# Kernel optimization log

Hardware: AMD Instinct MI355X
Metric: run time of the kernel (lower is better)

## Reference

```python
import jax, jax.numpy as jnp
import numpy as np

B, S, D, H = 8, 1024, 768, 12
DH = D // H
EPS = 1e-5
NEG = -1e9


def _layernorm(x, g, b):
    mu = jnp.mean(x, axis=-1, keepdims=True)
    var = jnp.mean((x - mu) ** 2, axis=-1, keepdims=True)
    return (x - mu) * jax.lax.rsqrt(var + EPS) * g + b


def setup_inputs() -> dict:
    key = jax.random.key(0)
    ks = jax.random.split(key, 20)
    sc = 0.02
    x = jax.random.normal(ks[0], (B, S, D), dtype=jnp.float32)
    src_mask = jax.random.randint(ks[1], (B, S), 0, 2) > 0
    # weights stored as (in, out): y = x @ W + b (same math as torch x @ W.T + b)
    Wq = jax.random.normal(ks[2], (D, D), jnp.float32) * sc
    bq = jnp.zeros((D,), jnp.float32)
    Wk = jax.random.normal(ks[3], (D, D), jnp.float32) * sc
    bk = jnp.zeros((D,), jnp.float32)
    Wv = jax.random.normal(ks[4], (D, D), jnp.float32) * sc
    bv = jnp.zeros((D,), jnp.float32)
    Wo = jax.random.normal(ks[5], (D, D), jnp.float32) * sc
    bo = jnp.zeros((D,), jnp.float32)
    g1 = jnp.ones((D,), jnp.float32)
    be1 = jnp.zeros((D,), jnp.float32)
    W1 = jax.random.normal(ks[6], (D, 2 * D), jnp.float32) * sc
    b1 = jnp.zeros((2 * D,), jnp.float32)
    W2 = jax.random.normal(ks[7], (2 * D, D), jnp.float32) * sc
    b2 = jnp.zeros((D,), jnp.float32)
    g2 = jnp.ones((D,), jnp.float32)
    be2 = jnp.zeros((D,), jnp.float32)
    return dict(x=x, src_mask=src_mask, Wq=Wq, bq=bq, Wk=Wk, bk=bk, Wv=Wv, bv=bv,
                Wo=Wo, bo=bo, g1=g1, be1=be1, W1=W1, b1=b1, W2=W2, b2=b2,
                g2=g2, be2=be2)


def reference(x, src_mask, Wq, bq, Wk, bk, Wv, bv, Wo, bo, g1, be1, W1, b1, W2, b2, g2, be2):
    # QKV projections, split into heads: [B, S, H, DH]
    q = (x @ Wq + bq).reshape(B, S, H, DH)
    k = (x @ Wk + bk).reshape(B, S, H, DH)
    v = (x @ Wv + bv).reshape(B, S, H, DH)
    # scores [B, H, S, S]; scale by sqrt(head_dim) as in original
    scores = jnp.einsum('bqhd,bkhd->bhqk', q, k) / np.sqrt(DH).astype(np.float32)
    # additive key mask broadcast over heads and queries
    mask = jnp.where(src_mask[:, None, None, :], 0.0, NEG).astype(scores.dtype)
    A = jax.nn.softmax(scores + mask, axis=-1)
    ctx = jnp.einsum('bhqk,bkhd->bqhd', A, v).reshape(B, S, D)
    attn_out = ctx @ Wo + bo + x
    h = _layernorm(attn_out, g1, be1)
    ff = jax.nn.relu(h @ W1 + b1) @ W2 + b2
    out = _layernorm(ff + h, g2, be2)
    return out
```

## Files before the change

kernel.cpp:

```cpp
#include <hip/hip_runtime.h>
#include <cstdint>
#include <cstddef>

typedef unsigned short u16;
typedef __attribute__((ext_vector_type(8))) __bf16 bf16x8;
typedef __attribute__((ext_vector_type(4))) float floatx4;

#define Bz 8
#define Sz 1024
#define Dz 768
#define Hz 12
#define DHz 64

__device__ __forceinline__ u16 f2b(float f) {
  unsigned u = __float_as_uint(f);
  return (u16)((u + 0x7fffu + ((u >> 16) & 1u)) >> 16);
}

__device__ __forceinline__ u16 f2b_hw(float f) {
  __bf16 h = (__bf16)f;
  return __builtin_bit_cast(u16, h);
}

__device__ __forceinline__ bf16x8 ld8(const u16* p) {
  union { uint4 u; bf16x8 b; } t;
  t.u = *reinterpret_cast<const uint4*>(p);
  return t.b;
}

__device__ __forceinline__ void load_lds16(const u16* g, u16* l) {
  __builtin_amdgcn_global_load_lds(
      (const __attribute__((address_space(1))) unsigned int*)g,
      (__attribute__((address_space(3))) unsigned int*)l, 16, 0, 0);
}

__global__ __launch_bounds__(256) void cvt4(const float* __restrict__ src,
                                            u16* __restrict__ dst, int n4) {
  int i = blockIdx.x * 256 + threadIdx.x;
  if (i >= n4) return;
  float4 v = reinterpret_cast<const float4*>(src)[i];
  union { u16 s[4]; uint2 u; } t;
  t.s[0] = f2b(v.x); t.s[1] = f2b(v.y); t.s[2] = f2b(v.z); t.s[3] = f2b(v.w);
  reinterpret_cast<uint2*>(dst)[i] = t.u;
}

__global__ __launch_bounds__(256)
void wtrans(const float* __restrict__ s0, const float* __restrict__ s1,
            const float* __restrict__ s2, u16* __restrict__ dst,
            int K, int N, int srcN) {
  __shared__ float T[32][33];
  const int tx = threadIdx.x & 31, ty = threadIdx.x >> 5;
  const int n0 = blockIdx.x * 32, k0 = blockIdx.y * 32;
  const int n = n0 + tx;
  const float* src = s0;
  int nn = n;
  if (s1 && n >= 1536) { src = s2; nn = n - 1536; }
  else if (s1 && n >= 768) { src = s1; nn = n - 768; }
#pragma unroll
  for (int i = 0; i < 4; ++i)
    T[ty + i * 8][tx] = src[(size_t)(k0 + ty + i * 8) * srcN + nn];
  __syncthreads();
#pragma unroll
  for (int i = 0; i < 4; ++i)
    dst[(size_t)(n0 + ty + i * 8) * K + k0 + tx] = f2b(T[tx][ty + i * 8]);
}

template <int EPI>
__global__ __launch_bounds__(256, 3)
void gemm_k(const u16* __restrict__ A, const u16* __restrict__ Bt,
            int M, int N, int K,
            const float* __restrict__ bias0, const float* __restrict__ resid,
            float* __restrict__ outF, u16* __restrict__ outB) {
  __shared__ __align__(16) u16 As[3][128 * 32];
  __shared__ __align__(16) u16 Bs[3][128 * 32];
  const int tid = threadIdx.x;
  const int lane = tid & 63, wave = tid >> 6;
  const int l15 = lane & 15, quad = lane >> 4;

  const int nx = gridDim.x;
  const int nwg = nx * gridDim.y;
  const int lin = blockIdx.y * nx + blockIdx.x;
  const int swz = (lin & 7) * (nwg >> 3) + (lin >> 3);
  const int bx = swz % nx, by = swz / nx;

  const int m0 = by * 128, n0 = bx * 128;
  const int wm = (wave >> 1) * 64, wn = (wave & 1) * 64;

  floatx4 acc[4][4];
#pragma unroll
  for (int i = 0; i < 4; ++i)
#pragma unroll
    for (int j = 0; j < 4; ++j) acc[i][j] = {0.f, 0.f, 0.f, 0.f};

  const int srow = lane >> 2;
  const int scol = (((lane & 3) ^ ((lane >> 3) & 3))) * 8;
  const u16* pA = A + (size_t)(m0 + wave * 32 + srow) * K + scol;
  const u16* pB = Bt + (size_t)(n0 + wave * 32 + srow) * K + scol;

#pragma unroll
  for (int t = 0; t < 2; ++t)
#pragma unroll
    for (int j = 0; j < 2; ++j) {
      load_lds16(pA + (size_t)(j * 16) * K + t * 32, &As[t][(wave * 2 + j) * 512]);
      load_lds16(pB + (size_t)(j * 16) * K + t * 32, &Bs[t][(wave * 2 + j) * 512]);
    }

  const int NIT = K >> 5;
  const int rsw = (l15 >> 1) & 3;
  int cur = 0;
  for (int i = 0; i < NIT; ++i) {
    if (i == NIT - 1) asm volatile("s_waitcnt vmcnt(0)" ::: "memory");
    else              asm volatile("s_waitcnt vmcnt(4)" ::: "memory");
    __builtin_amdgcn_s_barrier();
    bf16x8 af[4], bf[4];
#pragma unroll
    for (int ii = 0; ii < 4; ++ii)
      af[ii] = ld8(&As[cur][(wm + ii * 16 + l15) * 32 + (quad ^ rsw) * 8]);
#pragma unroll
    for (int j = 0; j < 4; ++j)
      bf[j] = ld8(&Bs[cur][(wn + j * 16 + l15) * 32 + (quad ^ rsw) * 8]);
    __builtin_amdgcn_sched_barrier(0);
    if (i + 2 < NIT) {
      const int k2 = (i + 2) << 5;
      int pf = cur + 2; if (pf >= 3) pf -= 3;
#pragma unroll
      for (int j = 0; j < 2; ++j) {
        load_lds16(pA + (size_t)(j * 16) * K + k2, &As[pf][(wave * 2 + j) * 512]);
        load_lds16(pB + (size_t)(j * 16) * K + k2, &Bs[pf][(wave * 2 + j) * 512]);
      }
    }
    __builtin_amdgcn_sched_barrier(0);
#pragma unroll
    for (int ii = 0; ii < 4; ++ii)
#pragma unroll
      for (int j = 0; j < 4; ++j)
        acc[ii][j] = __builtin_amdgcn_mfma_f32_16x16x32_bf16(af[ii], bf[j],
                                                             acc[ii][j], 0, 0, 0);
    cur += 1; if (cur == 3) cur = 0;
  }

#pragma unroll
  for (int i = 0; i < 4; ++i) {
    int mbase = m0 + wm + i * 16 + quad * 4;
#pragma unroll
    for (int j = 0; j < 4; ++j) {
      int n = n0 + wn + j * 16 + l15;
#pragma unroll
      for (int r = 0; r < 4; ++r) {
        int mm = mbase + r;
        float v = acc[i][j][r];
        if (EPI == 1) {
          v += bias0[n] + resid[(size_t)mm * N + n];
          outF[(size_t)mm * N + n] = v;
        } else {
          v += bias0[n];
          v = fmaxf(v, 0.f);
          outB[(size_t)mm * N + n] = f2b(v);
        }
      }
    }
  }
}

template <int EPI>
__global__ __launch_bounds__(256, 2)
void gemm_w(const u16* __restrict__ A, const u16* __restrict__ Bt,
            int M, int N, int K,
            const float* __restrict__ bias0, const float* __restrict__ bias1,
            const float* __restrict__ bias2,
            u16* __restrict__ outB,
            u16* __restrict__ qO, u16* __restrict__ kO, u16* __restrict__ vtO) {
  __shared__ __align__(16) u16 As[3][128 * 32];
  __shared__ __align__(16) u16 Bs[3][256 * 32];
  const int tid = threadIdx.x;
  const int lane = tid & 63, wave = tid >> 6;
  const int l15 = lane & 15, quad = lane >> 4;

  const int nx = gridDim.x;
  const int nwg = nx * gridDim.y;
  const int lin = blockIdx.y * nx + blockIdx.x;
  const int swz = (lin & 7) * (nwg >> 3) + (lin >> 3);
  const int bx = swz % nx, by = swz / nx;

  const int m0 = by * 128, n0 = bx * 256;

  floatx4 acc[8][4];
#pragma unroll
  for (int i = 0; i < 8; ++i)
#pragma unroll
    for (int j = 0; j < 4; ++j) acc[i][j] = {0.f, 0.f, 0.f, 0.f};

  const int srow = lane >> 2;
  const int scol = (((lane & 3) ^ ((lane >> 3) & 3))) * 8;
  const u16* pA = A + (size_t)(m0 + wave * 32 + srow) * K + scol;
  const u16* pB = Bt + (size_t)(n0 + wave * 64 + srow) * K + scol;

#pragma unroll
  for (int t = 0; t < 2; ++t) {
#pragma unroll
    for (int j = 0; j < 2; ++j)
      load_lds16(pA + (size_t)(j * 16) * K + t * 32,
                 &As[t][(wave * 2 + j) * 512]);
#pragma unroll
    for (int j = 0; j < 4; ++j)
      load_lds16(pB + (size_t)(j * 16) * K + t * 32,
                 &Bs[t][(wave * 4 + j) * 512]);
  }

  const int NIT = K >> 5;
  const int rsw = (l15 >> 1) & 3;
  int cur = 0;
  for (int i = 0; i < NIT; ++i) {
    if (i == NIT - 1) asm volatile("s_waitcnt vmcnt(0)" ::: "memory");
    else              asm volatile("s_waitcnt vmcnt(6)" ::: "memory");
    __builtin_amdgcn_s_barrier();
    bf16x8 af[8], bf[4];
#pragma unroll
    for (int mi = 0; mi < 8; ++mi)
      af[mi] = ld8(&As[cur][(mi * 16 + l15) * 32 + (quad ^ rsw) * 8]);
#pragma unroll
    for (int nj = 0; nj < 4; ++nj)
      bf[nj] = ld8(&Bs[cur][(wave * 64 + nj * 16 + l15) * 32 + (quad ^ rsw) * 8]);
    __builtin_amdgcn_sched_barrier(0);
    if (i + 2 < NIT) {
      const int k2 = (i + 2) << 5;
      int pf = cur + 2; if (pf >= 3) pf -= 3;
#pragma unroll
      for (int j = 0; j < 2; ++j)
        load_lds16(pA + (size_t)(j * 16) * K + k2, &As[pf][(wave * 2 + j) * 512]);
#pragma unroll
      for (int j = 0; j < 4; ++j)
        load_lds16(pB + (size_t)(j * 16) * K + k2, &Bs[pf][(wave * 4 + j) * 512]);
    }
    __builtin_amdgcn_sched_barrier(0);
#pragma unroll
    for (int mi = 0; mi < 8; ++mi)
#pragma unroll
      for (int nj = 0; nj < 4; ++nj)
        acc[mi][nj] = __builtin_amdgcn_mfma_f32_16x16x32_bf16(af[mi], bf[nj],
                                                              acc[mi][nj], 0, 0, 0);
    cur += 1; if (cur == 3) cur = 0;
  }

#pragma unroll
  for (int mi = 0; mi < 8; ++mi) {
    int mbase = m0 + mi * 16 + quad * 4;
#pragma unroll
    for (int nj = 0; nj < 4; ++nj) {
      int n = n0 + wave * 64 + nj * 16 + l15;
#pragma unroll
      for (int r = 0; r < 4; ++r) {
        int mm = mbase + r;
        float v = acc[mi][nj][r];
        if (EPI == 0) {
          if (n < 768) {
            v += bias0[n];
            qO[(size_t)mm * 768 + n] = f2b(v);
          } else if (n < 1536) {
            v += bias1[n - 768];
            kO[(size_t)mm * 768 + (n - 768)] = f2b(v);
          } else {
            int d = n - 1536;
            v += bias2[d];
            int hh = d >> 6, dh = d & 63;
            int bb = mm >> 10, ss = mm & 1023;
            vtO[((size_t)(bb * Hz + hh) * DHz + dh) * Sz + ss] = f2b(v);
          }
        } else {
          v += bias0[n];
          v = fmaxf(v, 0.f);
          outB[(size_t)mm * N + n] = f2b(v);
        }
      }
    }
  }
}

__global__ __launch_bounds__(256, 3)
void attn_k(const u16* __restrict__ q, const u16* __restrict__ kbuf,
            const u16* __restrict__ vt, const int* __restrict__ mask,
            u16* __restrict__ ctx) {
  __shared__ float addend[Sz];
  __shared__ __align__(16) u16 Ks[2][64 * 64];
  __shared__ __align__(16) u16 Vs[2][64 * 64];
  __shared__ __align__(16) u16 P[4][16][68];
  const int tid = threadIdx.x;
  const int wave = tid >> 6, lane = tid & 63;
  const int l15 = lane & 15, quad = lane >> 4;
  const int lin = blockIdx.y * 16 + blockIdx.x;
  const int swzid = (lin & 7) * 192 + (lin >> 3);
  const int bq = swzid & 15;
  const int bh = swzid >> 4;
  const int b = bh / Hz, h = bh - b * Hz;

  for (int s = tid; s < Sz; s += 256)
    addend[s] = mask[b * Sz + s] ? 0.f : -1e9f;

  const int qrow = bq * 64 + wave * 16 + l15;
  const u16* qp = q + (size_t)(b * Sz + qrow) * Dz + h * DHz;
  const bf16x8 fq0 = ld8(qp + quad * 8);
  const bf16x8 fq1 = ld8(qp + 32 + quad * 8);

  const int l7 = l15 & 7;
  const int s0q = quad ^ l7;

  const int srow = tid >> 3;
  const int spos = tid & 7;
  const int schunk = spos ^ (srow & 7);
  const u16* kg = kbuf + (size_t)(b * Sz + srow) * Dz + h * DHz + schunk * 8;
  const u16* vg = vt + (size_t)(b * Hz + h) * (DHz * Sz) + (size_t)srow * Sz +
                  schunk * 8;

  float m_l = -1e30f, l_l = 0.f;
  floatx4 o[4];
#pragma unroll
  for (int nt = 0; nt < 4; ++nt) o[nt] = {0.f, 0.f, 0.f, 0.f};

  load_lds16(kg, &Ks[0][wave * 512]);
  load_lds16(kg + (size_t)32 * Dz, &Ks[0][2048 + wave * 512]);
  load_lds16(vg, &Vs[0][wave * 512]);
  load_lds16(vg + (size_t)32 * Sz, &Vs[0][2048 + wave * 512]);

  for (int kt = 0; kt < 16; ++kt) {
    const int cur = kt & 1;
    asm volatile("s_waitcnt vmcnt(0)" ::: "memory");
    __builtin_amdgcn_s_barrier();
    bf16x8 fk0[4], fk1[4];
#pragma unroll
    for (int t = 0; t < 4; ++t) {
      const int krow = t * 16 + l15;
      fk0[t] = ld8(&Ks[cur][krow * 64 + s0q * 8]);
      fk1[t] = ld8(&Ks[cur][krow * 64 + (s0q ^ 4) * 8]);
    }
    __builtin_amdgcn_sched_barrier(0);
    if (kt + 1 < 16) {
      const size_t ko = (size_t)(kt + 1) * 64 * Dz;
      const int ve = (kt + 1) * 64;
      const int nb = cur ^ 1;
      load_lds16(kg + ko, &Ks[nb][wave * 512]);
      load_lds16(kg + ko + (size_t)32 * Dz, &Ks[nb][2048 + wave * 512]);
      load_lds16(vg + ve, &Vs[nb][wave * 512]);
      load_lds16(vg + ve + (size_t)32 * Sz, &Vs[nb][2048 + wave * 512]);
    }
    __builtin_amdgcn_sched_barrier(0);

    floatx4 z[4];
#pragma unroll
    for (int t = 0; t < 4; ++t) {
      floatx4 zz = {0.f, 0.f, 0.f, 0.f};
      zz = __builtin_amdgcn_mfma_f32_16x16x32_bf16(fk0[t], fq0, zz, 0, 0, 0);
      zz = __builtin_amdgcn_mfma_f32_16x16x32_bf16(fk1[t], fq1, zz, 0, 0, 0);
      const float4 ad =
          *reinterpret_cast<const float4*>(&addend[kt * 64 + t * 16 + quad * 4]);
      z[t][0] = zz[0] * 0.125f + ad.x;
      z[t][1] = zz[1] * 0.125f + ad.y;
      z[t][2] = zz[2] * 0.125f + ad.z;
      z[t][3] = zz[3] * 0.125f + ad.w;
    }
    float mx = fmaxf(fmaxf(z[0][0], z[0][1]), fmaxf(z[0][2], z[0][3]));
#pragma unroll
    for (int t = 1; t < 4; ++t)
      mx = fmaxf(mx, fmaxf(fmaxf(z[t][0], z[t][1]), fmaxf(z[t][2], z[t][3])));
    mx = fmaxf(mx, __shfl_xor(mx, 16, 64));
    mx = fmaxf(mx, __shfl_xor(mx, 32, 64));
    if (!__all(mx <= m_l + 8.f)) {
      const float nm = fmaxf(m_l, mx);
      const float alpha = __expf(m_l - nm);
      m_l = nm;
      l_l *= alpha;
      float av[4];
#pragma unroll
      for (int r = 0; r < 4; ++r) av[r] = __shfl(alpha, quad * 4 + r, 64);
#pragma unroll
      for (int nt = 0; nt < 4; ++nt)
#pragma unroll
        for (int r = 0; r < 4; ++r) o[nt][r] *= av[r];
    }
    float su = 0.f;
#pragma unroll
    for (int t = 0; t < 4; ++t) {
      union { u16 s[4]; uint2 u; } pk;
#pragma unroll
      for (int r = 0; r < 4; ++r) {
        float p = __expf(z[t][r] - m_l);
        su += p;
        pk.s[r] = f2b_hw(p);
      }
      *reinterpret_cast<uint2*>(&P[wave][l15][t * 16 + quad * 4]) = pk.u;
    }
    su += __shfl_xor(su, 16, 64);
    su += __shfl_xor(su, 32, 64);
    l_l += su;
    const bf16x8 ap0 = ld8(&P[wave][l15][quad * 8]);
    const bf16x8 ap1 = ld8(&P[wave][l15][32 + quad * 8]);
#pragma unroll
    for (int nt = 0; nt < 4; ++nt) {
      bf16x8 bv0 = ld8(&Vs[cur][(nt * 16 + l15) * 64 + ((quad ^ l7) * 8)]);
      bf16x8 bv1 = ld8(&Vs[cur][(nt * 16 + l15) * 64 + (((4 + quad) ^ l7) * 8)]);
      o[nt] = __builtin_amdgcn_mfma_f32_16x16x32_bf16(ap0, bv0, o[nt], 0, 0, 0);
      o[nt] = __builtin_amdgcn_mfma_f32_16x16x32_bf16(ap1, bv1, o[nt], 0, 0, 0);
    }
  }

  const float linv = 1.f / l_l;
  float lv[4];
#pragma unroll
  for (int r = 0; r < 4; ++r) lv[r] = __shfl(linv, quad * 4 + r, 64);
  const int qr = bq * 64 + wave * 16 + quad * 4;
#pragma unroll
  for (int nt = 0; nt < 4; ++nt)
#pragma unroll
    for (int r = 0; r < 4; ++r) {
      float v = o[nt][r] * lv[r];
      ctx[(size_t)(b * Sz + qr + r) * Dz + h * DHz + nt * 16 + l15] = f2b(v);
    }
}

__global__ __launch_bounds__(256)
void ln_k(const float* __restrict__ in, const float* __restrict__ g,
          const float* __restrict__ be, float* __restrict__ outF,
          u16* __restrict__ outB) {
  const int row = blockIdx.x;
  const float* x = in + (size_t)row * Dz;
  const int tid = threadIdx.x;
  float v0 = x[tid], v1 = x[tid + 256], v2 = x[tid + 512];
  float s = v0 + v1 + v2;
  float s2 = v0 * v0 + v1 * v1 + v2 * v2;
#pragma unroll
  for (int off = 1; off < 64; off <<= 1) {
    s += __shfl_xor(s, off, 64);
    s2 += __shfl_xor(s2, off, 64);
  }
  __shared__ float red[8];
  int wave = tid >> 6, lane = tid & 63;
  if (lane == 0) { red[wave] = s; red[4 + wave] = s2; }
  __syncthreads();
  s = red[0] + red[1] + red[2] + red[3];
  s2 = red[4] + red[5] + red[6] + red[7];
  const float mu = s * (1.f / 768.f);
  const float rstd = rsqrtf(s2 * (1.f / 768.f) - mu * mu + 1e-5f);
  float vv[3] = {v0, v1, v2};
#pragma unroll
  for (int e = 0; e < 3; ++e) {
    int col = tid + e * 256;
    float y = (vv[e] - mu) * rstd * g[col] + be[col];
    outF[(size_t)row * Dz + col] = y;
    if (outB) outB[(size_t)row * Dz + col] = f2b(y);
  }
}

extern "C" void kernel_launch(void* const* d_in, const int* in_sizes, int n_in,
                              void* d_out, int out_size, void* d_ws,
                              size_t ws_size, hipStream_t stream) {
  const float* x   = (const float*)d_in[0];
  const int*   msk = (const int*)d_in[1];
  const float* Wq  = (const float*)d_in[2];
  const float* bq  = (const float*)d_in[3];
  const float* Wk  = (const float*)d_in[4];
  const float* bk  = (const float*)d_in[5];
  const float* Wv  = (const float*)d_in[6];
  const float* bv  = (const float*)d_in[7];
  const float* Wo  = (const float*)d_in[8];
  const float* bo  = (const float*)d_in[9];
  const float* g1  = (const float*)d_in[10];
  const float* be1 = (const float*)d_in[11];
  const float* W1  = (const float*)d_in[12];
  const float* b1  = (const float*)d_in[13];
  const float* W2  = (const float*)d_in[14];
  const float* b2  = (const float*)d_in[15];
  const float* g2  = (const float*)d_in[16];
  const float* be2 = (const float*)d_in[17];
  float* out = (float*)d_out;

  char* ws = (char*)d_ws;
  u16*   xb    = (u16*)(ws + 0);
  u16*   wqkvb = (u16*)(ws + 12582912);
  u16*   wob   = (u16*)(ws + 16121856);
  u16*   w1b   = (u16*)(ws + 17301504);
  u16*   w2b   = (u16*)(ws + 19660800);
  u16*   qb    = (u16*)(ws + 22020096);
  u16*   kb    = (u16*)(ws + 34603008);
  u16*   vtb   = (u16*)(ws + 47185920);
  u16*   ctx   = (u16*)(ws + 59768832);
  float* att   = (float*)(ws + 72351744);
  float* hf    = (float*)(ws + 97517568);
  u16*   hb    = (u16*)(ws + 122683392);
  u16*   f1    = (u16*)(ws + 47185920);
  float* yy    = (float*)(ws + 22020096);

  cvt4<<<6291456 / 4 / 256, 256, 0, stream>>>(x, xb, 6291456 / 4);
  wtrans<<<dim3(2304 / 32, 768 / 32), 256, 0, stream>>>(Wq, Wk, Wv, wqkvb, 768,
                                                        2304, 768);
  wtrans<<<dim3(24, 24), 256, 0, stream>>>(Wo, nullptr, nullptr, wob, 768, 768,
                                           768);
  wtrans<<<dim3(48, 24), 256, 0, stream>>>(W1, nullptr, nullptr, w1b, 768, 1536,
                                           1536);
  wtrans<<<dim3(24, 48), 256, 0, stream>>>(W2, nullptr, nullptr, w2b, 1536, 768,
                                           768);

  gemm_w<0><<<dim3(2304 / 256, 8192 / 128), 256, 0, stream>>>(
      xb, wqkvb, 8192, 2304, 768, bq, bk, bv, nullptr, qb, kb, vtb);
  attn_k<<<dim3(Sz / 64, Bz * Hz), 256, 0, stream>>>(qb, kb, vtb, msk, ctx);
  gemm_k<1><<<dim3(768 / 128, 8192 / 128), 256, 0, stream>>>(
      ctx, wob, 8192, 768, 768, bo, x, att, nullptr);
  ln_k<<<8192, 256, 0, stream>>>(att, g1, be1, hf, hb);
  gemm_w<2><<<dim3(1536 / 256, 8192 / 128), 256, 0, stream>>>(
      hb, w1b, 8192, 1536, 768, b1, nullptr, nullptr, f1, nullptr, nullptr,
      nullptr);
  gemm_k<1><<<dim3(768 / 128, 8192 / 128), 256, 0, stream>>>(
      f1, w2b, 8192, 768, 1536, b2, hf, yy, nullptr);
  ln_k<<<8192, 256, 0, stream>>>(yy, g2, be2, out, nullptr);
}
```

Measured before the change: 376.7 us.

## Replace wide GEMM with 8-wave 256x256 tile kernel and interleaved prefetch schedule

Replaces the 4-wave 128x256 tile GEMM used for the QKV and FFN1 projections with an 8-wave 256x256 tile kernel. It uses a K-step of 64, double-buffered LDS with an XOR swizzle, and global-to-LDS loads split into stages interleaved between MFMA groups, with s_setprio to favour the matrix work. The larger tile raises arithmetic intensity and halves the grid in M. In exchange it uses 128KB of LDS per block, which limits occupancy, and the grid for 1536/2304-wide outputs becomes small (192 or 288 blocks) relative to the CU count.

```diff
diff --git a/kernel.cpp b/kernel.cpp
--- a/kernel.cpp
+++ b/kernel.cpp
@@ -163,26 +163,26 @@
 }
 
 template <int EPI>
-__global__ __launch_bounds__(256, 2)
-void gemm_w(const u16* __restrict__ A, const u16* __restrict__ Bt,
-            int M, int N, int K,
-            const float* __restrict__ bias0, const float* __restrict__ bias1,
-            const float* __restrict__ bias2,
-            u16* __restrict__ outB,
-            u16* __restrict__ qO, u16* __restrict__ kO, u16* __restrict__ vtO) {
-  __shared__ __align__(16) u16 As[3][128 * 32];
-  __shared__ __align__(16) u16 Bs[3][256 * 32];
+__global__ __launch_bounds__(512, 2)
+void gemm8(const u16* __restrict__ A, const u16* __restrict__ Bt,
+           int M, int N, int K,
+           const float* __restrict__ bias0, const float* __restrict__ bias1,
+           const float* __restrict__ bias2,
+           u16* __restrict__ outB,
+           u16* __restrict__ qO, u16* __restrict__ kO, u16* __restrict__ vtO) {
+  __shared__ __align__(16) u16 As[2][256 * 64];
+  __shared__ __align__(16) u16 Bs[2][256 * 64];
   const int tid = threadIdx.x;
   const int lane = tid & 63, wave = tid >> 6;
-  const int l15 = lane & 15, quad = lane >> 4;
+  const int l15 = lane & 15, quad = lane >> 4, l7 = lane & 7;
+  const int wr = wave >> 2, wc = wave & 3;
 
   const int nx = gridDim.x;
   const int nwg = nx * gridDim.y;
   const int lin = blockIdx.y * nx + blockIdx.x;
   const int swz = (lin & 7) * (nwg >> 3) + (lin >> 3);
   const int bx = swz % nx, by = swz / nx;
-
-  const int m0 = by * 128, n0 = bx * 256;
+  const int m0 = by * 256, n0 = bx * 256;
 
   floatx4 acc[8][4];
 #pragma unroll
@@ -190,64 +190,132 @@
 #pragma unroll
     for (int j = 0; j < 4; ++j) acc[i][j] = {0.f, 0.f, 0.f, 0.f};
 
-  const int srow = lane >> 2;
-  const int scol = (((lane & 3) ^ ((lane >> 3) & 3))) * 8;
-  const u16* pA = A + (size_t)(m0 + wave * 32 + srow) * K + scol;
-  const u16* pB = Bt + (size_t)(n0 + wave * 64 + srow) * K + scol;
-
-#pragma unroll
-  for (int t = 0; t < 2; ++t) {
-#pragma unroll
-    for (int j = 0; j < 2; ++j)
-      load_lds16(pA + (size_t)(j * 16) * K + t * 32,
-                 &As[t][(wave * 2 + j) * 512]);
-#pragma unroll
-    for (int j = 0; j < 4; ++j)
-      load_lds16(pB + (size_t)(j * 16) * K + t * 32,
-                 &Bs[t][(wave * 4 + j) * 512]);
-  }
-
-  const int NIT = K >> 5;
-  const int rsw = (l15 >> 1) & 3;
-  int cur = 0;
-  for (int i = 0; i < NIT; ++i) {
-    if (i == NIT - 1) asm volatile("s_waitcnt vmcnt(0)" ::: "memory");
-    else              asm volatile("s_waitcnt vmcnt(6)" ::: "memory");
+  const int schunk = (lane & 7) ^ ((lane >> 3) & 7);
+  const u16* pA = A + (size_t)(m0 + wave * 16 + (lane >> 3)) * K + schunk * 8;
+  const u16* pB = Bt + (size_t)(n0 + wave * 16 + (lane >> 3)) * K + schunk * 8;
+
+  const int NT = K >> 6;
+
+#define STAGE8(c, T, s)                                                        \
+  {                                                                            \
+    const int hOff = ((s) & 1) * 128;                                          \
+    if ((s) < 2) {                                                             \
+      load_lds16(pA + (size_t)hOff * K + (size_t)(T) * 64,                     \
+                 &As[c][(hOff + wave * 16) * 64]);                             \
+      load_lds16(pA + (size_t)(hOff + 8) * K + (size_t)(T) * 64,               \
+                 &As[c][(hOff + wave * 16 + 8) * 64]);                         \
+    } else {                                                                   \
+      load_lds16(pB + (size_t)hOff * K + (size_t)(T) * 64,                     \
+                 &Bs[c][(hOff + wave * 16) * 64]);                             \
+      load_lds16(pB + (size_t)(hOff + 8) * K + (size_t)(T) * 64,               \
+                 &Bs[c][(hOff + wave * 16 + 8) * 64]);                         \
+    }                                                                          \
+  }
+
+#pragma unroll
+  for (int s = 0; s < 4; ++s) STAGE8(0, 0, s);
+#pragma unroll
+  for (int s = 0; s < 3; ++s) STAGE8(1, 1, s);
+
+  bf16x8 bfr[4][2], afA[2][2], afB[2][2];
+
+  for (int t = 0; t < NT; ++t) {
+    const int c = t & 1;
+    if (t == NT - 1) asm volatile("s_waitcnt vmcnt(0)" ::: "memory");
+    else             asm volatile("s_waitcnt vmcnt(6)" ::: "memory");
     __builtin_amdgcn_s_barrier();
-    bf16x8 af[8], bf[4];
-#pragma unroll
-    for (int mi = 0; mi < 8; ++mi)
-      af[mi] = ld8(&As[cur][(mi * 16 + l15) * 32 + (quad ^ rsw) * 8]);
+
 #pragma unroll
     for (int nj = 0; nj < 4; ++nj)
-      bf[nj] = ld8(&Bs[cur][(wave * 64 + nj * 16 + l15) * 32 + (quad ^ rsw) * 8]);
-    __builtin_amdgcn_sched_barrier(0);
-    if (i + 2 < NIT) {
-      const int k2 = (i + 2) << 5;
-      int pf = cur + 2; if (pf >= 3) pf -= 3;
-#pragma unroll
-      for (int j = 0; j < 2; ++j)
-        load_lds16(pA + (size_t)(j * 16) * K + k2, &As[pf][(wave * 2 + j) * 512]);
-#pragma unroll
-      for (int j = 0; j < 4; ++j)
-        load_lds16(pB + (size_t)(j * 16) * K + k2, &Bs[pf][(wave * 4 + j) * 512]);
-    }
-    __builtin_amdgcn_sched_barrier(0);
-#pragma unroll
-    for (int mi = 0; mi < 8; ++mi)
+#pragma unroll
+      for (int kk = 0; kk < 2; ++kk)
+        bfr[nj][kk] = ld8(&Bs[c][(wc * 64 + nj * 16 + l15) * 64 +
+                                 (((kk * 4 + quad) ^ l7) * 8)]);
+#pragma unroll
+    for (int m2 = 0; m2 < 2; ++m2)
+#pragma unroll
+      for (int kk = 0; kk < 2; ++kk) {
+        afA[m2][kk] = ld8(&As[c][(wr * 128 + (0 + m2) * 16 + l15) * 64 +
+                                 (((kk * 4 + quad) ^ l7) * 8)]);
+        afB[m2][kk] = ld8(&As[c][(wr * 128 + (2 + m2) * 16 + l15) * 64 +
+                                 (((kk * 4 + quad) ^ l7) * 8)]);
+      }
+    __builtin_amdgcn_sched_barrier(0);
+    if (t + 1 < NT) STAGE8(c ^ 1, t + 1, 3);
+    __builtin_amdgcn_sched_barrier(0);
+
+    __builtin_amdgcn_s_setprio(1);
+#pragma unroll
+    for (int m2 = 0; m2 < 2; ++m2)
 #pragma unroll
       for (int nj = 0; nj < 4; ++nj)
-        acc[mi][nj] = __builtin_amdgcn_mfma_f32_16x16x32_bf16(af[mi], bf[nj],
-                                                              acc[mi][nj], 0, 0, 0);
-    cur += 1; if (cur == 3) cur = 0;
-  }
+#pragma unroll
+        for (int kk = 0; kk < 2; ++kk)
+          acc[m2][nj] = __builtin_amdgcn_mfma_f32_16x16x32_bf16(
+              afA[m2][kk], bfr[nj][kk], acc[m2][nj], 0, 0, 0);
+    __builtin_amdgcn_s_setprio(0);
+#pragma unroll
+    for (int m2 = 0; m2 < 2; ++m2)
+#pragma unroll
+      for (int kk = 0; kk < 2; ++kk)
+        afA[m2][kk] = ld8(&As[c][(wr * 128 + (4 + m2) * 16 + l15) * 64 +
+                                 (((kk * 4 + quad) ^ l7) * 8)]);
+    __builtin_amdgcn_s_setprio(1);
+#pragma unroll
+    for (int m2 = 0; m2 < 2; ++m2)
+#pragma unroll
+      for (int nj = 0; nj < 4; ++nj)
+#pragma unroll
+        for (int kk = 0; kk < 2; ++kk)
+          acc[2 + m2][nj] = __builtin_amdgcn_mfma_f32_16x16x32_bf16(
+              afB[m2][kk], bfr[nj][kk], acc[2 + m2][nj], 0, 0, 0);
+    __builtin_amdgcn_s_setprio(0);
+#pragma unroll
+    for (int m2 = 0; m2 < 2; ++m2)
+#pragma unroll
+      for (int kk = 0; kk < 2; ++kk)
+        afB[m2][kk] = ld8(&As[c][(wr * 128 + (6 + m2) * 16 + l15) * 64 +
+                                 (((kk * 4 + quad) ^ l7) * 8)]);
+
+    asm volatile("s_waitcnt lgkmcnt(0)" ::: "memory");
+    __builtin_amdgcn_s_barrier();
+
+    const bool pf = (t + 2 < NT);
+    if (pf) STAGE8(c, t + 2, 0);
+    __builtin_amdgcn_sched_barrier(0);
+    __builtin_amdgcn_s_setprio(1);
+#pragma unroll
+    for (int m2 = 0; m2 < 2; ++m2)
+#pragma unroll
+      for (int nj = 0; nj < 4; ++nj)
+#pragma unroll
+        for (int kk = 0; kk < 2; ++kk)
+          acc[4 + m2][nj] = __builtin_amdgcn_mfma_f32_16x16x32_bf16(
+              afA[m2][kk], bfr[nj][kk], acc[4 + m2][nj], 0, 0, 0);
+    __builtin_amdgcn_s_setprio(0);
+    if (pf) STAGE8(c, t + 2, 1);
+    __builtin_amdgcn_sched_barrier(0);
+    __builtin_amdgcn_s_setprio(1);
+#pragma unroll
+    for (int m2 = 0; m2 < 2; ++m2)
+#pragma unroll
+      for (int nj = 0; nj < 4; ++nj)
+#pragma unroll
+        for (int kk = 0; kk < 2; ++kk)
+          acc[6 + m2][nj] = __builtin_amdgcn_mfma_f32_16x16x32_bf16(
+              afB[m2][kk], bfr[nj][kk], acc[6 + m2][nj], 0, 0, 0);
+    __builtin_amdgcn_s_setprio(0);
+    if (pf) STAGE8(c, t + 2, 2);
+    __builtin_amdgcn_sched_barrier(0);
+  }
+#undef STAGE8
 
 #pragma unroll
   for (int mi = 0; mi < 8; ++mi) {
-    int mbase = m0 + mi * 16 + quad * 4;
+    int mbase = m0 + wr * 128 + mi * 16 + quad * 4;
 #pragma unroll
     for (int nj = 0; nj < 4; ++nj) {
-      int n = n0 + wave * 64 + nj * 16 + l15;
+      int n = n0 + wc * 64 + nj * 16 + l15;
 #pragma unroll
       for (int r = 0; r < 4; ++r) {
         int mm = mbase + r;
@@ -498,13 +566,13 @@
   wtrans<<<dim3(24, 48), 256, 0, stream>>>(W2, nullptr, nullptr, w2b, 1536, 768,
                                            768);
 
-  gemm_w<0><<<dim3(2304 / 256, 8192 / 128), 256, 0, stream>>>(
+  gemm8<0><<<dim3(2304 / 256, 8192 / 256), 512, 0, stream>>>(
       xb, wqkvb, 8192, 2304, 768, bq, bk, bv, nullptr, qb, kb, vtb);
   attn_k<<<dim3(Sz / 64, Bz * Hz), 256, 0, stream>>>(qb, kb, vtb, msk, ctx);
   gemm_k<1><<<dim3(768 / 128, 8192 / 128), 256, 0, stream>>>(
       ctx, wob, 8192, 768, 768, bo, x, att, nullptr);
   ln_k<<<8192, 256, 0, stream>>>(att, g1, be1, hf, hb);
-  gemm_w<2><<<dim3(1536 / 256, 8192 / 128), 256, 0, stream>>>(
+  gemm8<2><<<dim3(1536 / 256, 8192 / 256), 512, 0, stream>>>(
       hb, w1b, 8192, 1536, 768, b1, nullptr, nullptr, f1, nullptr, nullptr,
       nullptr);
   gemm_k<1><<<dim3(768 / 128, 8192 / 128), 256, 0, stream>>>(
```

Result: slower. 394.3 us (+4.7%).

## Replace wide GEMM with 256x256-tile 8-wave kernel using K=64 staged pipeline

Applied to the files above, without the earlier changes.

The QKV and FFN1 GEMMs move from a 128x256 tile with 4 waves and a triple-buffered K=32 pipeline to a 256x256 tile with 8 waves (2x4 layout) and a double-buffered K=64 pipeline. Global-to-LDS staging is split into quarter-steps interleaved with the MFMA groups, with s_setprio raised around the MFMAs. The LDS swizzle becomes an XOR over 8 chunks. The aim is higher arithmetic intensity per tile and better overlap of loads with compute. In exchange the kernel uses 128KB of LDS per block and adds many barriers, and the grid is halved, which may cut occupancy and leave CUs underfilled (288 and 192 blocks).

```diff
diff --git a/kernel.cpp b/kernel.cpp
--- a/kernel.cpp
+++ b/kernel.cpp
@@ -11,6 +11,8 @@
 #define Dz 768
 #define Hz 12
 #define DHz 64
+
+#define SB0 __builtin_amdgcn_sched_barrier(0)
 
 __device__ __forceinline__ u16 f2b(float f) {
   unsigned u = __float_as_uint(f);
@@ -119,7 +121,7 @@
 #pragma unroll
     for (int j = 0; j < 4; ++j)
       bf[j] = ld8(&Bs[cur][(wn + j * 16 + l15) * 32 + (quad ^ rsw) * 8]);
-    __builtin_amdgcn_sched_barrier(0);
+    SB0;
     if (i + 2 < NIT) {
       const int k2 = (i + 2) << 5;
       int pf = cur + 2; if (pf >= 3) pf -= 3;
@@ -129,7 +131,7 @@
         load_lds16(pB + (size_t)(j * 16) * K + k2, &Bs[pf][(wave * 2 + j) * 512]);
       }
     }
-    __builtin_amdgcn_sched_barrier(0);
+    SB0;
 #pragma unroll
     for (int ii = 0; ii < 4; ++ii)
 #pragma unroll
@@ -163,26 +165,26 @@
 }
 
 template <int EPI>
-__global__ __launch_bounds__(256, 2)
-void gemm_w(const u16* __restrict__ A, const u16* __restrict__ Bt,
-            int M, int N, int K,
-            const float* __restrict__ bias0, const float* __restrict__ bias1,
-            const float* __restrict__ bias2,
-            u16* __restrict__ outB,
-            u16* __restrict__ qO, u16* __restrict__ kO, u16* __restrict__ vtO) {
-  __shared__ __align__(16) u16 As[3][128 * 32];
-  __shared__ __align__(16) u16 Bs[3][256 * 32];
+__global__ __launch_bounds__(512, 2)
+void gemm8(const u16* __restrict__ A, const u16* __restrict__ Bt,
+           int M, int N, int K,
+           const float* __restrict__ bias0, const float* __restrict__ bias1,
+           const float* __restrict__ bias2,
+           u16* __restrict__ outB,
+           u16* __restrict__ qO, u16* __restrict__ kO, u16* __restrict__ vtO) {
+  __shared__ __align__(16) u16 As[2][256 * 64];
+  __shared__ __align__(16) u16 Bs[2][256 * 64];
   const int tid = threadIdx.x;
   const int lane = tid & 63, wave = tid >> 6;
-  const int l15 = lane & 15, quad = lane >> 4;
+  const int l15 = lane & 15, quad = lane >> 4, l7 = lane & 7;
+  const int wr = wave >> 2, wc = wave & 3;
 
   const int nx = gridDim.x;
   const int nwg = nx * gridDim.y;
   const int lin = blockIdx.y * nx + blockIdx.x;
   const int swz = (lin & 7) * (nwg >> 3) + (lin >> 3);
   const int bx = swz % nx, by = swz / nx;
-
-  const int m0 = by * 128, n0 = bx * 256;
+  const int m0 = by * 256, n0 = bx * 256;
 
   floatx4 acc[8][4];
 #pragma unroll
@@ -190,64 +192,94 @@
 #pragma unroll
     for (int j = 0; j < 4; ++j) acc[i][j] = {0.f, 0.f, 0.f, 0.f};
 
-  const int srow = lane >> 2;
-  const int scol = (((lane & 3) ^ ((lane >> 3) & 3))) * 8;
-  const u16* pA = A + (size_t)(m0 + wave * 32 + srow) * K + scol;
-  const u16* pB = Bt + (size_t)(n0 + wave * 64 + srow) * K + scol;
-
-#pragma unroll
-  for (int t = 0; t < 2; ++t) {
-#pragma unroll
-    for (int j = 0; j < 2; ++j)
-      load_lds16(pA + (size_t)(j * 16) * K + t * 32,
-                 &As[t][(wave * 2 + j) * 512]);
-#pragma unroll
-    for (int j = 0; j < 4; ++j)
-      load_lds16(pB + (size_t)(j * 16) * K + t * 32,
-                 &Bs[t][(wave * 4 + j) * 512]);
-  }
-
-  const int NIT = K >> 5;
-  const int rsw = (l15 >> 1) & 3;
-  int cur = 0;
-  for (int i = 0; i < NIT; ++i) {
-    if (i == NIT - 1) asm volatile("s_waitcnt vmcnt(0)" ::: "memory");
-    else              asm volatile("s_waitcnt vmcnt(6)" ::: "memory");
-    __builtin_amdgcn_s_barrier();
-    bf16x8 af[8], bf[4];
-#pragma unroll
-    for (int mi = 0; mi < 8; ++mi)
-      af[mi] = ld8(&As[cur][(mi * 16 + l15) * 32 + (quad ^ rsw) * 8]);
-#pragma unroll
-    for (int nj = 0; nj < 4; ++nj)
-      bf[nj] = ld8(&Bs[cur][(wave * 64 + nj * 16 + l15) * 32 + (quad ^ rsw) * 8]);
-    __builtin_amdgcn_sched_barrier(0);
-    if (i + 2 < NIT) {
-      const int k2 = (i + 2) << 5;
-      int pf = cur + 2; if (pf >= 3) pf -= 3;
-#pragma unroll
-      for (int j = 0; j < 2; ++j)
-        load_lds16(pA + (size_t)(j * 16) * K + k2, &As[pf][(wave * 2 + j) * 512]);
-#pragma unroll
-      for (int j = 0; j < 4; ++j)
-        load_lds16(pB + (size_t)(j * 16) * K + k2, &Bs[pf][(wave * 4 + j) * 512]);
-    }
-    __builtin_amdgcn_sched_barrier(0);
-#pragma unroll
-    for (int mi = 0; mi < 8; ++mi)
-#pragma unroll
-      for (int nj = 0; nj < 4; ++nj)
-        acc[mi][nj] = __builtin_amdgcn_mfma_f32_16x16x32_bf16(af[mi], bf[nj],
-                                                              acc[mi][nj], 0, 0, 0);
-    cur += 1; if (cur == 3) cur = 0;
-  }
+  const int schunk = (lane & 7) ^ ((lane >> 3) & 7);
+  const u16* pA = A + (size_t)(m0 + wave * 16 + (lane >> 3)) * K + schunk * 8;
+  const u16* pB = Bt + (size_t)(n0 + wave * 16 + (lane >> 3)) * K + schunk * 8;
+
+  const int NT = K >> 6;
+
+#define STG_A(buf, T, hf)                                                      \
+  do {                                                                         \
+    load_lds16(pA + (size_t)((hf) * 128) * K + (size_t)(T) * 64,               \
+               &As[buf][(((hf) * 128) + wave * 16) * 64]);                     \
+    load_lds16(pA + (size_t)((hf) * 128 + 8) * K + (size_t)(T) * 64,           \
+               &As[buf][(((hf) * 128) + wave * 16 + 8) * 64]);                 \
+  } while (0)
+#define STG_B(buf, T, hf)                                                      \
+  do {                                                                         \
+    load_lds16(pB + (size_t)((hf) * 128) * K + (size_t)(T) * 64,               \
+               &Bs[buf][(((hf) * 128) + wave * 16) * 64]);                     \
+    load_lds16(pB + (size_t)((hf) * 128 + 8) * K + (size_t)(T) * 64,           \
+               &Bs[buf][(((hf) * 128) + wave * 16 + 8) * 64]);                 \
+  } while (0)
+
+  STG_B(0, 0, 0); STG_B(0, 0, 1); STG_A(0, 0, 0); STG_A(0, 0, 1);
+  STG_B(1, 1, 0); STG_B(1, 1, 1); STG_A(1, 1, 0);
+  asm volatile("s_waitcnt vmcnt(6)" ::: "memory");
+  __builtin_amdgcn_s_barrier();
+
+  bf16x8 bfr[4][2];
+
+  for (int t = 0; t < NT; ++t) {
+    const int c = t & 1;
+#pragma unroll
+    for (int q = 0; q < 4; ++q) {
+      bf16x8 af[2][2];
+      if (q == 0) {
+#pragma unroll
+        for (int nj = 0; nj < 4; ++nj)
+#pragma unroll
+          for (int kk = 0; kk < 2; ++kk)
+            bfr[nj][kk] = ld8(&Bs[c][(wc * 64 + nj * 16 + l15) * 64 +
+                                     (((kk * 4 + quad) ^ l7) * 8)]);
+      }
+#pragma unroll
+      for (int m2 = 0; m2 < 2; ++m2)
+#pragma unroll
+        for (int kk = 0; kk < 2; ++kk)
+          af[m2][kk] = ld8(&As[c][(wr * 128 + (q * 2 + m2) * 16 + l15) * 64 +
+                                  (((kk * 4 + quad) ^ l7) * 8)]);
+      SB0;
+      if (q == 0) {
+        if (t + 1 < NT) STG_A(c ^ 1, t + 1, 1);
+      } else if (q == 1) {
+        if (t + 2 < NT) STG_B(c, t + 2, 0);
+      } else if (q == 2) {
+        if (t + 2 < NT) STG_B(c, t + 2, 1);
+      } else {
+        if (t + 2 < NT) STG_A(c, t + 2, 0);
+      }
+      SB0;
+      if (q == 3) {
+        if (t >= NT - 2) asm volatile("s_waitcnt vmcnt(0)" ::: "memory");
+        else             asm volatile("s_waitcnt vmcnt(6)" ::: "memory");
+      }
+      __builtin_amdgcn_s_barrier();
+      asm volatile("s_waitcnt lgkmcnt(0)" ::: "memory");
+      SB0;
+      __builtin_amdgcn_s_setprio(1);
+#pragma unroll
+      for (int m2 = 0; m2 < 2; ++m2)
+#pragma unroll
+        for (int nj = 0; nj < 4; ++nj)
+#pragma unroll
+          for (int kk = 0; kk < 2; ++kk)
+            acc[q * 2 + m2][nj] = __builtin_amdgcn_mfma_f32_16x16x32_bf16(
+                af[m2][kk], bfr[nj][kk], acc[q * 2 + m2][nj], 0, 0, 0);
+      __builtin_amdgcn_s_setprio(0);
+      SB0;
+      __builtin_amdgcn_s_barrier();
+    }
+  }
+#undef STG_A
+#undef STG_B
 
 #pragma unroll
   for (int mi = 0; mi < 8; ++mi) {
-    int mbase = m0 + mi * 16 + quad * 4;
+    int mbase = m0 + wr * 128 + mi * 16 + quad * 4;
 #pragma unroll
     for (int nj = 0; nj < 4; ++nj) {
-      int n = n0 + wave * 64 + nj * 16 + l15;
+      int n = n0 + wc * 64 + nj * 16 + l15;
 #pragma unroll
       for (int r = 0; r < 4; ++r) {
         int mm = mbase + r;
@@ -332,7 +364,7 @@
       fk0[t] = ld8(&Ks[cur][krow * 64 + s0q * 8]);
       fk1[t] = ld8(&Ks[cur][krow * 64 + (s0q ^ 4) * 8]);
     }
-    __builtin_amdgcn_sched_barrier(0);
+    SB0;
     if (kt + 1 < 16) {
       const size_t ko = (size_t)(kt + 1) * 64 * Dz;
       const int ve = (kt + 1) * 64;
@@ -342,7 +374,7 @@
       load_lds16(vg + ve, &Vs[nb][wave * 512]);
       load_lds16(vg + ve + (size_t)32 * Sz, &Vs[nb][2048 + wave * 512]);
     }
-    __builtin_amdgcn_sched_barrier(0);
+    SB0;
 
     floatx4 z[4];
 #pragma unroll
@@ -498,13 +530,13 @@
   wtrans<<<dim3(24, 48), 256, 0, stream>>>(W2, nullptr, nullptr, w2b, 1536, 768,
                                            768);
 
-  gemm_w<0><<<dim3(2304 / 256, 8192 / 128), 256, 0, stream>>>(
+  gemm8<0><<<dim3(2304 / 256, 8192 / 256), 512, 0, stream>>>(
       xb, wqkvb, 8192, 2304, 768, bq, bk, bv, nullptr, qb, kb, vtb);
   attn_k<<<dim3(Sz / 64, Bz * Hz), 256, 0, stream>>>(qb, kb, vtb, msk, ctx);
   gemm_k<1><<<dim3(768 / 128, 8192 / 128), 256, 0, stream>>>(
       ctx, wob, 8192, 768, 768, bo, x, att, nullptr);
   ln_k<<<8192, 256, 0, stream>>>(att, g1, be1, hf, hb);
-  gemm_w<2><<<dim3(1536 / 256, 8192 / 128), 256, 0, stream>>>(
+  gemm8<2><<<dim3(1536 / 256, 8192 / 256), 512, 0, stream>>>(
       hb, w1b, 8192, 1536, 768, b1, nullptr, nullptr, f1, nullptr, nullptr,
       nullptr);
   gemm_k<1><<<dim3(768 / 128, 8192 / 128), 256, 0, stream>>>(
```

Result: slower. 397.8 us (+5.6%).
